# Kernel tuning notes

Measured on AMD Instinct MI355X. Metric: run time of the kernel, lower is better.

Reference implementation:

```python
import jax, jax.numpy as jnp
import numpy as np

BS = 16
CTX_PER = 1024   # local context nodes per proof state
ARGS_PER = 32    # arguments per proof state
KEY_DIM = 128
D_MODEL = 512


def setup_inputs() -> dict:
    key = jax.random.key(0)
    k1, k2, k3 = jax.random.split(key, 3)
    n_ctx = BS * CTX_PER
    n_args = BS * ARGS_PER
    # segment ids: sorted, uniform segments (static ragged structure)
    ctx_ids = jnp.repeat(jnp.arange(BS, dtype=jnp.int32), CTX_PER)
    arg_ids = jnp.repeat(jnp.arange(BS, dtype=jnp.int32), ARGS_PER)
    arg_values = jax.random.normal(k1, (n_args, KEY_DIM), dtype=jnp.float32)
    ctx_values = jax.random.normal(k2, (n_ctx, D_MODEL), dtype=jnp.float32)
    W = jax.random.normal(k3, (D_MODEL, KEY_DIM), dtype=jnp.float32) / np.sqrt(D_MODEL)
    b = jnp.zeros((KEY_DIM,), dtype=jnp.float32)
    return {"bs": BS, "arg_ids": arg_ids, "ctx_ids": ctx_ids,
            "arg_values": arg_values, "ctx_values": ctx_values, "W": W, "b": b}


def reference(bs, arg_ids, ctx_ids, arg_values, ctx_values, W, b):
    n_args = arg_ids.shape[0]
    n_ctx = ctx_ids.shape[0]
    # total (arg, ctx-element) pairs; static because segments are uniform by construction
    P = n_args * (n_ctx // bs)

    # ctx_lens[s] = number of context elements in proof state s
    ctx_lens = jax.ops.segment_sum(jnp.ones_like(ctx_ids), ctx_ids, num_segments=bs)
    arg_ctx_lens = ctx_lens[arg_ids]                      # [n_args]

    # ragged-range construction: row id + within-row offset for each flat pair
    arg_ends = jnp.cumsum(arg_ctx_lens)                   # inclusive cumsum
    arg_starts = arg_ends - arg_ctx_lens                  # exclusive cumsum
    pos = jnp.arange(P, dtype=arg_ends.dtype)
    rows = jnp.searchsorted(arg_ends, pos, side='right')  # value_rowids  [P]
    offs = pos - arg_starts[rows]                         # ragged range values [P]

    # column index into flat context values
    ctx_starts = jnp.cumsum(ctx_lens) - ctx_lens          # exclusive cumsum [bs]
    cols = ctx_starts[arg_ids[rows]] + offs               # [P]

    keys_all = ctx_values @ W + b                         # Dense key projection [n_ctx, key_dim]
    queries = arg_values[rows]                            # [P, key_dim]
    keys = keys_all[cols]                                 # [P, key_dim]
    logits_flat = jnp.einsum('pd,pd->p', queries, keys)   # [P]
    return rows.astype(jnp.int32), logits_flat
```

## Files before the change

kernel.cpp:

```cpp
#include <hip/hip_runtime.h>


#define BSZ        16
#define CTX_PER    1024
#define ARGS_PER   32
#define KD         128
#define DM         512
#define N_ARGS     (BSZ * ARGS_PER)
#define P_TOTAL    (N_ARGS * CTX_PER)

typedef __attribute__((ext_vector_type(8))) short short8;
typedef __attribute__((ext_vector_type(4))) float float4v;

__device__ inline short bf16_of(float x) {
    unsigned u = __builtin_bit_cast(unsigned, x);
    unsigned r = (u + 0x7fffu + ((u >> 16) & 1u)) >> 16;
    return (short)r;
}

__device__ inline short8 cvt8(float4 lo, float4 hi) {
    short8 r;
    r[0] = bf16_of(lo.x); r[1] = bf16_of(lo.y); r[2] = bf16_of(lo.z); r[3] = bf16_of(lo.w);
    r[4] = bf16_of(hi.x); r[5] = bf16_of(hi.y); r[6] = bf16_of(hi.z); r[7] = bf16_of(hi.w);
    return r;
}

__global__ __launch_bounds__(256) void qproj_kernel(
    const float* __restrict__ arg, const float* __restrict__ W,
    const float* __restrict__ b, short* __restrict__ Qp, float* __restrict__ qb)
{
    const int t = threadIdx.x, lane = t & 63, wave = t >> 6;
    const int mtile = blockIdx.x >> 3;
    const int ntile = (blockIdx.x & 7) * 4 + wave;
    const int n = lane & 15, quad = lane >> 4;

    const float* asrc = arg + (size_t)(mtile * 16 + n) * KD + quad * 8;
    short8 afr[4];
    #pragma unroll
    for (int kt = 0; kt < 4; ++kt)
        afr[kt] = cvt8(*(const float4*)(asrc + kt * 32), *(const float4*)(asrc + kt * 32 + 4));

    const float* wsrc = W + (size_t)(ntile * 16 + n) * KD + quad * 8;
    float4v acc = {0.f, 0.f, 0.f, 0.f};
    #pragma unroll
    for (int kt = 0; kt < 4; ++kt) {
        short8 bfr = cvt8(*(const float4*)(wsrc + kt * 32), *(const float4*)(wsrc + kt * 32 + 4));
        acc = __builtin_amdgcn_mfma_f32_16x16x32_bf16(afr[kt], bfr, acc, 0, 0, 0);
    }
    #pragma unroll
    for (int r = 0; r < 4; ++r)
        Qp[(size_t)(mtile * 16 + quad * 4 + r) * DM + ntile * 16 + n] = bf16_of(acc[r]);

    if ((blockIdx.x & 7) == 0) {
        __shared__ float red[16][17];
        const int al = t >> 4, seg = t & 15;
        const float* qrow = arg + (size_t)(mtile * 16 + al) * KD + seg * 8;
        float p = 0.f;
        #pragma unroll
        for (int j = 0; j < 8; ++j) p += qrow[j] * b[seg * 8 + j];
        red[al][seg] = p;
        __syncthreads();
        if (t < 16) {
            float ssum = 0.f;
            #pragma unroll
            for (int j = 0; j < 16; ++j) ssum += red[t][j];
            qb[mtile * 16 + t] = ssum;
        }
    }
}

__global__ __launch_bounds__(256, 3) void main_kernel(
    const float* __restrict__ ctx, const short* __restrict__ Qp,
    const float* __restrict__ qb, float* __restrict__ out)
{
    __shared__ __align__(16) short Qpl[32][520];
    __shared__ __align__(16) short Cxl[16][520];

    const int t = threadIdx.x, lane = t & 63, wave = t >> 6;
    const int s = blockIdx.x >> 6;
    const int chunk = blockIdx.x & 63;

    const short* qsrc = Qp + (size_t)s * 32 * DM;
    #pragma unroll
    for (int i = 0; i < 8; ++i) {
        const int u = i * 256 + t;
        const int row = u >> 6, c = u & 63;
        *(float4*)&Qpl[row][c * 8] = *(const float4*)(qsrc + (size_t)row * DM + c * 8);
    }
    const float* csrc = ctx + (size_t)(s * CTX_PER + chunk * 16) * DM;
    #pragma unroll
    for (int i = 0; i < 4; ++i) {
        const int u = i * 256 + t;
        const int row = u >> 6, c8 = u & 63;
        const float4 lo = *(const float4*)(csrc + (size_t)row * DM + c8 * 8);
        const float4 hi = *(const float4*)(csrc + (size_t)row * DM + c8 * 8 + 4);
        *(short8*)&Cxl[row][c8 * 8] = cvt8(lo, hi);
    }
    __syncthreads();

    const int n = lane & 15, quad = lane >> 4;
    const int k0 = wave * 128;

    float4v acc0 = {0.f, 0.f, 0.f, 0.f};
    float4v acc1 = {0.f, 0.f, 0.f, 0.f};
    #pragma unroll
    for (int kt = 0; kt < 4; ++kt) {
        short8 bfr = *(const short8*)&Cxl[n][k0 + kt * 32 + quad * 8];
        short8 a0  = *(const short8*)&Qpl[n][k0 + kt * 32 + quad * 8];
        short8 a1  = *(const short8*)&Qpl[16 + n][k0 + kt * 32 + quad * 8];
        acc0 = __builtin_amdgcn_mfma_f32_16x16x32_bf16(a0, bfr, acc0, 0, 0, 0);
        acc1 = __builtin_amdgcn_mfma_f32_16x16x32_bf16(a1, bfr, acc1, 0, 0, 0);
    }

    __syncthreads();
    float* Sp = (float*)&Qpl[0][0];
    #pragma unroll
    for (int r = 0; r < 4; ++r) {
        Sp[wave * 512 + (quad * 4 + r) * 16 + n]      = acc0[r];
        Sp[wave * 512 + (16 + quad * 4 + r) * 16 + n] = acc1[r];
    }
    __syncthreads();

    const int a = t >> 3, c2 = (t & 7) * 2;
    const int base = a * 16 + c2;
    float v0 = Sp[base]     + Sp[512 + base]     + Sp[1024 + base]     + Sp[1536 + base];
    float v1 = Sp[base + 1] + Sp[512 + base + 1] + Sp[1024 + base + 1] + Sp[1536 + base + 1];
    const int ga = s * ARGS_PER + a;
    const float qbv = qb[ga];
    const size_t off = (size_t)ga * CTX_PER + chunk * 16 + c2;
    *(float2*)(out + P_TOTAL + off) = make_float2(v0 + qbv, v1 + qbv);
    *(float2*)(out + off)           = make_float2((float)ga, (float)ga);
}

extern "C" void kernel_launch(void* const* d_in, const int* in_sizes, int n_in,
                              void* d_out, int out_size, void* d_ws, size_t ws_size,
                              hipStream_t stream)
{
    const float* arg_values = (const float*)d_in[3];
    const float* ctx_values = (const float*)d_in[4];
    const float* W          = (const float*)d_in[5];
    const float* b          = (const float*)d_in[6];
    float* out = (float*)d_out;

    short* Qp = (short*)d_ws;
    float* qb = (float*)((char*)d_ws + (size_t)N_ARGS * DM * sizeof(short));

    qproj_kernel<<<256, 256, 0, stream>>>(arg_values, W, b, Qp, qb);
    main_kernel<<<BSZ * 64, 256, 0, stream>>>(ctx_values, Qp, qb, out);
}
```

Baseline: 91.30 us.

## Stream context rows straight into MFMA fragments and drop cross-wave K-split reduction

The main kernel no longer stages converted context rows in shared memory. Each wave instead owns a 16-arg by 16-ctx output tile and loops over the full K dimension, loading and converting fp32 context directly from global memory into bf16 MFMA operands. This removes the shared-memory K-split partial-sum reduction and its extra barriers, and halves the block count, with each block covering 32 context rows. Each context row is now read twice, once per arg-half wave, and output stores become scattered 4-byte writes rather than float2 writes. Occupancy bounds are also lowered.

```diff
diff --git a/kernel.cpp b/kernel.cpp
--- a/kernel.cpp
+++ b/kernel.cpp
@@ -69,16 +69,26 @@
     }
 }
 
-__global__ __launch_bounds__(256, 3) void main_kernel(
+__global__ __launch_bounds__(256, 2) void main_kernel(
     const float* __restrict__ ctx, const short* __restrict__ Qp,
     const float* __restrict__ qb, float* __restrict__ out)
 {
     __shared__ __align__(16) short Qpl[32][520];
-    __shared__ __align__(16) short Cxl[16][520];
 
     const int t = threadIdx.x, lane = t & 63, wave = t >> 6;
-    const int s = blockIdx.x >> 6;
-    const int chunk = blockIdx.x & 63;
+    const int s = blockIdx.x >> 5;
+    const int chunk = blockIdx.x & 31;
+
+    const int n = lane & 15, quad = lane >> 4;
+    const int A16 = (wave & 1) * 16;
+    const int rowbase = chunk * 32 + ((wave >> 1) & 1) * 16;
+
+    const float* csrc = ctx + (size_t)(s * CTX_PER + rowbase + n) * DM + quad * 8;
+
+    const float4 c0lo = *(const float4*)(csrc);
+    const float4 c0hi = *(const float4*)(csrc + 4);
+    const float4 c1lo = *(const float4*)(csrc + 32);
+    const float4 c1hi = *(const float4*)(csrc + 36);
 
     const short* qsrc = Qp + (size_t)s * 32 * DM;
     #pragma unroll
@@ -87,49 +97,42 @@
         const int row = u >> 6, c = u & 63;
         *(float4*)&Qpl[row][c * 8] = *(const float4*)(qsrc + (size_t)row * DM + c * 8);
     }
-    const float* csrc = ctx + (size_t)(s * CTX_PER + chunk * 16) * DM;
-    #pragma unroll
-    for (int i = 0; i < 4; ++i) {
-        const int u = i * 256 + t;
-        const int row = u >> 6, c8 = u & 63;
-        const float4 lo = *(const float4*)(csrc + (size_t)row * DM + c8 * 8);
-        const float4 hi = *(const float4*)(csrc + (size_t)row * DM + c8 * 8 + 4);
-        *(short8*)&Cxl[row][c8 * 8] = cvt8(lo, hi);
-    }
-    __syncthreads();
 
-    const int n = lane & 15, quad = lane >> 4;
-    const int k0 = wave * 128;
-
-    float4v acc0 = {0.f, 0.f, 0.f, 0.f};
-    float4v acc1 = {0.f, 0.f, 0.f, 0.f};
-    #pragma unroll
-    for (int kt = 0; kt < 4; ++kt) {
-        short8 bfr = *(const short8*)&Cxl[n][k0 + kt * 32 + quad * 8];
-        short8 a0  = *(const short8*)&Qpl[n][k0 + kt * 32 + quad * 8];
-        short8 a1  = *(const short8*)&Qpl[16 + n][k0 + kt * 32 + quad * 8];
-        acc0 = __builtin_amdgcn_mfma_f32_16x16x32_bf16(a0, bfr, acc0, 0, 0, 0);
-        acc1 = __builtin_amdgcn_mfma_f32_16x16x32_bf16(a1, bfr, acc1, 0, 0, 0);
+    {
+        const int a = t >> 3, c4 = (t & 7) * 4;
+        const int ga = s * ARGS_PER + a;
+        const float gaf = (float)ga;
+        float4 rv = make_float4(gaf, gaf, gaf, gaf);
+        *(float4*)(out + (size_t)ga * CTX_PER + chunk * 32 + c4) = rv;
     }
 
     __syncthreads();
-    float* Sp = (float*)&Qpl[0][0];
+
+    const short* qrow = &Qpl[A16 + n][quad * 8];
+
+    float4v acc = {0.f, 0.f, 0.f, 0.f};
+    {
+        short8 a0 = *(const short8*)(qrow);
+        acc = __builtin_amdgcn_mfma_f32_16x16x32_bf16(a0, cvt8(c0lo, c0hi), acc, 0, 0, 0);
+        short8 a1 = *(const short8*)(qrow + 32);
+        acc = __builtin_amdgcn_mfma_f32_16x16x32_bf16(a1, cvt8(c1lo, c1hi), acc, 0, 0, 0);
+    }
     #pragma unroll
-    for (int r = 0; r < 4; ++r) {
-        Sp[wave * 512 + (quad * 4 + r) * 16 + n]      = acc0[r];
-        Sp[wave * 512 + (16 + quad * 4 + r) * 16 + n] = acc1[r];
+    for (int kt = 2; kt < 16; ++kt) {
+        const float4 lo = *(const float4*)(csrc + kt * 32);
+        const float4 hi = *(const float4*)(csrc + kt * 32 + 4);
+        short8 bfr = cvt8(lo, hi);
+        short8 a  = *(const short8*)(qrow + kt * 32);
+        acc = __builtin_amdgcn_mfma_f32_16x16x32_bf16(a, bfr, acc, 0, 0, 0);
     }
-    __syncthreads();
 
-    const int a = t >> 3, c2 = (t & 7) * 2;
-    const int base = a * 16 + c2;
-    float v0 = Sp[base]     + Sp[512 + base]     + Sp[1024 + base]     + Sp[1536 + base];
-    float v1 = Sp[base + 1] + Sp[512 + base + 1] + Sp[1024 + base + 1] + Sp[1536 + base + 1];
-    const int ga = s * ARGS_PER + a;
-    const float qbv = qb[ga];
-    const size_t off = (size_t)ga * CTX_PER + chunk * 16 + c2;
-    *(float2*)(out + P_TOTAL + off) = make_float2(v0 + qbv, v1 + qbv);
-    *(float2*)(out + off)           = make_float2((float)ga, (float)ga);
+    const int ga0 = s * ARGS_PER + A16 + quad * 4;
+    const float4 qv = *(const float4*)(qb + ga0);
+    float* obase = out + P_TOTAL + (size_t)ga0 * CTX_PER + rowbase + n;
+    obase[0]           = acc[0] + qv.x;
+    obase[CTX_PER]     = acc[1] + qv.y;
+    obase[2 * CTX_PER] = acc[2] + qv.z;
+    obase[3 * CTX_PER] = acc[3] + qv.w;
 }
 
 extern "C" void kernel_launch(void* const* d_in, const int* in_sizes, int n_in,
@@ -146,5 +149,5 @@
     float* qb = (float*)((char*)d_ws + (size_t)N_ARGS * DM * sizeof(short));
 
     qproj_kernel<<<256, 256, 0, stream>>>(arg_values, W, b, Qp, qb);
-    main_kernel<<<BSZ * 64, 256, 0, stream>>>(ctx_values, Qp, qb, out);
+    main_kernel<<<BSZ * 32, 256, 0, stream>>>(ctx_values, Qp, qb, out);
 }
```

New measurement: 93.55 us. 2.5% more time.

## Load MFMA fragments directly from global memory, dropping LDS staging

Applied to the files above, without the earlier changes.

The main kernel now loads the context rows and projected queries straight from global memory into registers in MFMA fragment layout. This removes the LDS staging buffers and the first barrier, and converts to bf16 in registers just before the MFMAs. The smaller shared footprint allows the occupancy hint to rise from 3 to 4 blocks per CU, and cvt8 now uses the packed HIP float2-to-bf16 intrinsic. The trade-off is that each lane's global loads are less coalesced (32-byte pieces per row) and more registers are held live.

```diff
diff --git a/kernel.cpp b/kernel.cpp
--- a/kernel.cpp
+++ b/kernel.cpp
@@ -1,4 +1,5 @@
 #include <hip/hip_runtime.h>
+#include <hip/hip_bf16.h>
 
 
 #define BSZ        16
@@ -19,10 +20,12 @@
 }
 
 __device__ inline short8 cvt8(float4 lo, float4 hi) {
-    short8 r;
-    r[0] = bf16_of(lo.x); r[1] = bf16_of(lo.y); r[2] = bf16_of(lo.z); r[3] = bf16_of(lo.w);
-    r[4] = bf16_of(hi.x); r[5] = bf16_of(hi.y); r[6] = bf16_of(hi.z); r[7] = bf16_of(hi.w);
-    return r;
+    union { short8 s; __hip_bfloat162 h[4]; } u;
+    u.h[0] = __float22bfloat162_rn(make_float2(lo.x, lo.y));
+    u.h[1] = __float22bfloat162_rn(make_float2(lo.z, lo.w));
+    u.h[2] = __float22bfloat162_rn(make_float2(hi.x, hi.y));
+    u.h[3] = __float22bfloat162_rn(make_float2(hi.z, hi.w));
+    return u.s;
 }
 
 __global__ __launch_bounds__(256) void qproj_kernel(
@@ -69,51 +72,44 @@
     }
 }
 
-__global__ __launch_bounds__(256, 3) void main_kernel(
+__global__ __launch_bounds__(256, 4) void main_kernel(
     const float* __restrict__ ctx, const short* __restrict__ Qp,
     const float* __restrict__ qb, float* __restrict__ out)
 {
-    __shared__ __align__(16) short Qpl[32][520];
-    __shared__ __align__(16) short Cxl[16][520];
+    __shared__ float Sp[4 * 512];
 
     const int t = threadIdx.x, lane = t & 63, wave = t >> 6;
     const int s = blockIdx.x >> 6;
     const int chunk = blockIdx.x & 63;
 
-    const short* qsrc = Qp + (size_t)s * 32 * DM;
-    #pragma unroll
-    for (int i = 0; i < 8; ++i) {
-        const int u = i * 256 + t;
-        const int row = u >> 6, c = u & 63;
-        *(float4*)&Qpl[row][c * 8] = *(const float4*)(qsrc + (size_t)row * DM + c * 8);
-    }
-    const float* csrc = ctx + (size_t)(s * CTX_PER + chunk * 16) * DM;
-    #pragma unroll
-    for (int i = 0; i < 4; ++i) {
-        const int u = i * 256 + t;
-        const int row = u >> 6, c8 = u & 63;
-        const float4 lo = *(const float4*)(csrc + (size_t)row * DM + c8 * 8);
-        const float4 hi = *(const float4*)(csrc + (size_t)row * DM + c8 * 8 + 4);
-        *(short8*)&Cxl[row][c8 * 8] = cvt8(lo, hi);
-    }
-    __syncthreads();
-
     const int n = lane & 15, quad = lane >> 4;
     const int k0 = wave * 128;
+
+    const float* csrc = ctx + (size_t)(s * CTX_PER + chunk * 16 + n) * DM + k0 + quad * 8;
+    float4 clo[4], chi[4];
+    #pragma unroll
+    for (int kt = 0; kt < 4; ++kt) {
+        clo[kt] = *(const float4*)(csrc + kt * 32);
+        chi[kt] = *(const float4*)(csrc + kt * 32 + 4);
+    }
+
+    const short* qsrc = Qp + (size_t)(s * 32 + n) * DM + k0 + quad * 8;
+    short8 a0[4], a1[4];
+    #pragma unroll
+    for (int kt = 0; kt < 4; ++kt) {
+        a0[kt] = *(const short8*)(qsrc + kt * 32);
+        a1[kt] = *(const short8*)(qsrc + 16 * DM + kt * 32);
+    }
 
     float4v acc0 = {0.f, 0.f, 0.f, 0.f};
     float4v acc1 = {0.f, 0.f, 0.f, 0.f};
     #pragma unroll
     for (int kt = 0; kt < 4; ++kt) {
-        short8 bfr = *(const short8*)&Cxl[n][k0 + kt * 32 + quad * 8];
-        short8 a0  = *(const short8*)&Qpl[n][k0 + kt * 32 + quad * 8];
-        short8 a1  = *(const short8*)&Qpl[16 + n][k0 + kt * 32 + quad * 8];
-        acc0 = __builtin_amdgcn_mfma_f32_16x16x32_bf16(a0, bfr, acc0, 0, 0, 0);
-        acc1 = __builtin_amdgcn_mfma_f32_16x16x32_bf16(a1, bfr, acc1, 0, 0, 0);
+        short8 bfr = cvt8(clo[kt], chi[kt]);
+        acc0 = __builtin_amdgcn_mfma_f32_16x16x32_bf16(a0[kt], bfr, acc0, 0, 0, 0);
+        acc1 = __builtin_amdgcn_mfma_f32_16x16x32_bf16(a1[kt], bfr, acc1, 0, 0, 0);
     }
 
-    __syncthreads();
-    float* Sp = (float*)&Qpl[0][0];
     #pragma unroll
     for (int r = 0; r < 4; ++r) {
         Sp[wave * 512 + (quad * 4 + r) * 16 + n]      = acc0[r];
```

Result: slower. 95.13 us (+4.2%).
